# Kernel optimization log

Hardware: AMD Instinct MI355X
Metric: run time of the kernel (lower is better)

The kernel has to match this reference:

```python
import jax, jax.numpy as jnp
import numpy as np

# sizes
B, NA, DEG, TPE = 128, 32, 16, 4
N = B * NA            # 4096 atoms
E = N * DEG           # 65536 edges
T = E * TPE           # 262144 triplets
EA, EE, DT = 128, 128, 64   # atom emb, edge emb, triplet bottleneck
NR, NS, NB = 64, 16, 3      # radial basis, spherical basis, blocks
LAT, HID, NC = 128, 256, 230
CUTOFF, NTYPES = 7.0, 100


def _lattice(lengths, angles):
    """Crystallographic lengths[B,3]/angles[B,3] (deg) -> lattice matrix [B,3,3]."""
    a, b, c = lengths[:, 0], lengths[:, 1], lengths[:, 2]
    al, be, ga = (jnp.deg2rad(angles[:, i]) for i in range(3))
    cos_al, cos_be, cos_ga = jnp.cos(al), jnp.cos(be), jnp.cos(ga)
    sin_ga = jnp.sin(ga)
    zero = jnp.zeros_like(a)
    v1 = jnp.stack([a, zero, zero], -1)
    v2 = jnp.stack([b * cos_ga, b * sin_ga, zero], -1)
    cx = cos_be
    cy = (cos_al - cos_be * cos_ga) / sin_ga
    cz = jnp.sqrt(jnp.clip(1.0 - cx * cx - cy * cy, 1e-8))
    v3 = jnp.stack([c * cx, c * cy, c * cz], -1)
    return jnp.stack([v1, v2, v3], 1)


def setup_inputs() -> dict:
    key = jax.random.key(0)
    ks = jax.random.split(key, 32)

    def w(i, shape, scale=1.0):
        fan_in = shape[-2]
        return scale * jax.random.normal(ks[i], shape, jnp.float32) / np.sqrt(fan_in)

    inp = {
        "noise_levels": jax.random.uniform(ks[0], (B, 1), jnp.float32),
        "frac_coords": jax.random.uniform(ks[1], (N, 3), jnp.float32),
        "lengths": 5.0 + 5.0 * jax.random.uniform(ks[2], (B, 3), jnp.float32),
        "angles": 60.0 + 60.0 * jax.random.uniform(ks[3], (B, 3), jnp.float32),
        "atom_types": jax.random.randint(ks[4], (N,), 0, NTYPES),
        "num_atoms": jnp.full((B,), NA, dtype=jnp.int32),
    }
    # per-crystal random radius graph (no self loops)
    src_l = jax.random.randint(ks[5], (B, NA * DEG), 0, NA)
    dst_l = (src_l + jax.random.randint(ks[6], (B, NA * DEG), 1, NA)) % NA
    off = (jnp.arange(B) * NA)[:, None]
    inp["edge_index"] = jnp.stack([(src_l + off).reshape(-1), (dst_l + off).reshape(-1)]).astype(jnp.int32)
    inp["id3_ji"] = jax.random.randint(ks[7], (T,), 0, E)
    inp["id3_kj"] = jax.random.randint(ks[8], (T,), 0, E)
    # parameters
    inp["atom_emb"] = jax.random.normal(ks[9], (NTYPES, EA), jnp.float32)
    inp["W_hz"] = w(10, (EA + 1, EA))
    inp["W_edge"] = w(11, (2 * EA + NR, EE))
    inp["Wm"] = w(12, (NB, EE, EE))
    inp["Wr1"] = w(13, (NB, NR, EE))
    inp["Wdown"] = w(14, (NB, EE, DT))
    inp["Wcbf"] = w(15, (NB, NS, DT))
    inp["Wup"] = w(16, (NB, DT, EE), 0.5)
    inp["Wa"] = w(17, (NB, EE, EA))
    inp["Wr2"] = w(18, (NB, NR, EA))
    inp["Wh"] = w(19, (NB, EA, EA), 0.5)
    inp["Ws"] = w(20, (NB, EA, EE), 0.5)
    inp["Wt"] = w(21, (NB, EA, EE), 0.5)
    inp["W_out"] = w(22, (EA, LAT))
    inp["W_fc0"] = w(23, (LAT, HID)); inp["b_fc0"] = jnp.zeros((HID,), jnp.float32)
    inp["W_fc1"] = w(24, (HID, HID)); inp["b_fc1"] = jnp.zeros((HID,), jnp.float32)
    inp["W_fc2"] = w(25, (HID, NC)); inp["b_fc2"] = jnp.zeros((NC,), jnp.float32)
    return inp


def reference(noise_levels, frac_coords, lengths, angles, atom_emb, W_hz, W_edge,
              Wm, Wr1, Wdown, Wcbf, Wup, Wa, Wr2, Wh, Ws, Wt, W_out,
              W_fc0, b_fc0, W_fc1, b_fc1, W_fc2, b_fc2,
              atom_types, num_atoms, edge_index, id3_ji, id3_kj):
    silu, seg = jax.nn.silu, jax.ops.segment_sum
    batch = jnp.repeat(jnp.arange(B), num_atoms, total_repeat_length=N)  # [N]
    lat = _lattice(lengths, angles)                                      # [B,3,3]
    pos = jnp.einsum('ni,nij->nj', frac_coords, lat[batch])              # cart coords [N,3]
    src, dst = edge_index[0], edge_index[1]
    vec = pos[dst] - pos[src]                                            # [E,3]
    d = jnp.sqrt(jnp.sum(vec * vec, -1) + 1e-12)
    ds = d / CUTOFF
    # polynomial envelope (p=5) * Bessel radial basis
    env = jnp.where(ds < 1.0, 1.0 - 21.0 * ds**5 + 35.0 * ds**6 - 15.0 * ds**7, 0.0)
    n = jnp.arange(1, NR + 1, dtype=jnp.float32)
    rbf = env[:, None] * np.float32(np.sqrt(2.0 / CUTOFF)) * jnp.sin(n * jnp.pi * ds[:, None]) / d[:, None]  # [E,NR]
    # triplet angles and cosine basis
    v1, v2 = vec[id3_ji], vec[id3_kj]
    cosang = jnp.sum(v1 * v2, -1) / (jnp.linalg.norm(v1, axis=-1) * jnp.linalg.norm(v2, axis=-1) + 1e-9)
    ang = jnp.arccos(jnp.clip(cosang, -1.0 + 1e-6, 1.0 - 1e-6))
    cbf = jnp.cos(jnp.arange(NS, dtype=jnp.float32) * ang[:, None])      # [T,NS]
    # atom embedding conditioned on per-crystal noise level (z, latent_dim=1)
    h = silu(jnp.concatenate([atom_emb[atom_types], noise_levels[batch]], -1) @ W_hz)   # [N,EA]
    m = silu(jnp.concatenate([h[src], h[dst], rbf], -1) @ W_edge)                        # [E,EE]
    for b in range(NB):  # interaction blocks
        x = (silu(m @ Wm[b]) * (rbf @ Wr1[b])) @ Wdown[b]                # [E,DT]
        t = x[id3_kj] * (cbf @ Wcbf[b])                                  # gather + angular modulation [T,DT]
        m = m + silu(seg(t, id3_ji, num_segments=E) @ Wup[b])            # scatter triplets -> edges
        a = seg(silu(m @ Wa[b]) * (rbf @ Wr2[b]), dst, num_segments=N)   # scatter edges -> atoms
        h = h + silu(a @ Wh[b])
        m = m + silu(h[src] @ Ws[b] + h[dst] @ Wt[b])                    # re-embed edges from atoms
    z = seg(h @ W_out, batch, num_segments=B) / num_atoms[:, None].astype(h.dtype)  # [B,LAT] mean pool
    x = jax.nn.relu(z @ W_fc0 + b_fc0)
    x = jax.nn.relu(x @ W_fc1 + b_fc1)
    return x @ W_fc2 + b_fc2                                             # logits [B,NC]
```

## Files before the change

### kernel.cpp

```cpp
#include <hip/hip_runtime.h>
#include <hip/hip_bf16.h>
#include <math.h>

constexpr int B_ = 128, N_ = 4096, E_ = 65536, T_ = 262144;

typedef __attribute__((ext_vector_type(8))) __bf16 bf16x8;
typedef __attribute__((ext_vector_type(4))) float f32x4;
typedef __hip_bfloat16 bf16;

__device__ __forceinline__ float silu_f(float x){ return x / (1.0f + __expf(-x)); }
__device__ __forceinline__ float bf2f(bf16 v){ return __bfloat162float(v); }
__device__ __forceinline__ bf16  f2bf(float v){ return __float2bfloat16(v); }
__device__ __forceinline__ float bfx(bf16x8 v, int j){ __bf16 t = v[j]; return (float)t; }
__device__ __forceinline__ int   swz(int row, int col){ return col ^ ((row & 7) << 3); }

__global__ void hist2_kernel(const int* __restrict__ ji, const int* __restrict__ eidst,
                             int* __restrict__ cnt_ji, int* __restrict__ cnt_dst){
  int i = blockIdx.x*256 + threadIdx.x;
  if(i < T_) atomicAdd(&cnt_ji[ji[i]], 1);
  else       atomicAdd(&cnt_dst[eidst[i - T_]], 1);
}
__global__ void fill2_kernel(const int* __restrict__ ji, const int* __restrict__ eidst,
                             int* __restrict__ cur_ji, int* __restrict__ list_ji,
                             int* __restrict__ cur_dst, int* __restrict__ list_dst){
  int i = blockIdx.x*256 + threadIdx.x;
  if(i < T_){ int p = atomicAdd(&cur_ji[ji[i]], 1); list_ji[p] = i; }
  else { int e = i - T_; int p = atomicAdd(&cur_dst[eidst[e]], 1); list_dst[p] = e; }
}

__global__ __launch_bounds__(256) void scanA_kernel(const int* __restrict__ cnt_ji, const int* __restrict__ cnt_dst,
                                                    int* __restrict__ bsum){
  int blk = blockIdx.x;
  const int* src = (blk < 64) ? cnt_ji : cnt_dst;
  int base = (blk < 64) ? blk*1024 : (blk - 64)*1024;
  int t = threadIdx.x;
  int4 v = *(const int4*)&src[base + t*4];
  int s = v.x + v.y + v.z + v.w;
  #pragma unroll
  for(int d = 1; d < 64; d <<= 1) s += __shfl_xor(s, d);
  __shared__ int ws[4];
  if((t & 63) == 0) ws[t >> 6] = s;
  __syncthreads();
  if(t == 0) bsum[blk] = ws[0] + ws[1] + ws[2] + ws[3];
}
__global__ __launch_bounds__(128) void scanB_kernel(const int* __restrict__ bsum, int* __restrict__ boff){
  __shared__ int sh[68];
  int t = threadIdx.x;
  if(t < 68) sh[t] = bsum[t];
  __syncthreads();
  if(t == 0){
    int run = 0;
    for(int i = 0; i < 64; i++){ boff[i] = run; run += sh[i]; }
    run = 0;
    for(int i = 64; i < 68; i++){ boff[i] = run; run += sh[i]; }
  }
}
__global__ __launch_bounds__(256) void scanC_kernel(const int* __restrict__ cnt_ji, const int* __restrict__ cnt_dst,
                                                    const int* __restrict__ boff,
                                                    int* __restrict__ off_ji, int* __restrict__ cur_ji,
                                                    int* __restrict__ off_dst, int* __restrict__ cur_dst){
  int blk = blockIdx.x;
  const int* src; int* offs; int* cur; int base;
  if(blk < 64){ src = cnt_ji; offs = off_ji; cur = cur_ji; base = blk*1024; }
  else        { src = cnt_dst; offs = off_dst; cur = cur_dst; base = (blk - 64)*1024; }
  int t = threadIdx.x, lane = t & 63, w = t >> 6;
  int4 v = *(const int4*)&src[base + t*4];
  int s4 = v.x + v.y + v.z + v.w;
  int x = s4;
  #pragma unroll
  for(int d = 1; d < 64; d <<= 1){ int u = __shfl_up(x, d); if(lane >= d) x += u; }
  __shared__ int ws[4];
  if(lane == 63) ws[w] = x;
  __syncthreads();
  int wo = 0;
  for(int i = 0; i < w; i++) wo += ws[i];
  int o0 = boff[blk] + wo + (x - s4);
  int4 oo;
  oo.x = o0; oo.y = o0 + v.x; oo.z = oo.y + v.y; oo.w = oo.z + v.z;
  *(int4*)&offs[base + t*4] = oo;
  *(int4*)&cur[base + t*4]  = oo;
  if(blk == 0 && t == 0){ off_ji[E_] = T_; off_dst[N_] = E_; }
}

__global__ void pos_kernel(const float* __restrict__ frac, const float* __restrict__ lengths,
                           const float* __restrict__ angles, float* __restrict__ pos){
  int i = blockIdx.x*256 + threadIdx.x;
  if(i >= N_) return;
  int b = i >> 5;
  const float d2r = 0.017453292519943295f;
  float La = lengths[b*3+0], Lb = lengths[b*3+1], Lc = lengths[b*3+2];
  float al = angles[b*3+0]*d2r, be = angles[b*3+1]*d2r, ga = angles[b*3+2]*d2r;
  float ca = cosf(al), cb = cosf(be), cg = cosf(ga), sg = sinf(ga);
  float cx = cb, cy = (ca - cb*cg) / sg;
  float cz = sqrtf(fmaxf(1.0f - cx*cx - cy*cy, 1e-8f));
  float l00 = La, l10 = Lb*cg, l11 = Lb*sg, l20 = Lc*cx, l21 = Lc*cy, l22 = Lc*cz;
  float fx = frac[i*3], fy = frac[i*3+1], fz = frac[i*3+2];
  pos[i*3+0] = fx*l00 + fy*l10 + fz*l20;
  pos[i*3+1] = fy*l11 + fz*l21;
  pos[i*3+2] = fz*l22;
}

__global__ __launch_bounds__(256) void edge_kernel(const float* __restrict__ pos, const int* __restrict__ ei,
                                                   float* __restrict__ vec, bf16* __restrict__ rbf){
  int e = blockIdx.x*4 + (threadIdx.x >> 6);
  int lane = threadIdx.x & 63;
  int s = ei[e], d = ei[E_ + e];
  float vx = pos[d*3+0]-pos[s*3+0];
  float vy = pos[d*3+1]-pos[s*3+1];
  float vz = pos[d*3+2]-pos[s*3+2];
  float dd = sqrtf(vx*vx + vy*vy + vz*vz + 1e-12f);
  float dsc = dd * (1.0f/7.0f);
  float env = 0.0f;
  if(dsc < 1.0f){
    float d2 = dsc*dsc, d5 = d2*d2*dsc;
    env = 1.0f - 21.0f*d5 + 35.0f*d5*dsc - 15.0f*d5*d2;
  }
  float arg = (float)(lane+1) * 3.14159265358979f * dsc;
  rbf[(size_t)e*64 + lane] = f2bf(env * 0.5345224838248488f * sinf(arg) / dd);
  if(lane < 3){ vec[e*3+lane] = (lane==0) ? vx : (lane==1 ? vy : vz); }
}

__global__ __launch_bounds__(256) void tprep_kernel(const int* __restrict__ list, const int* __restrict__ ji,
                                                    const int* __restrict__ kj, const float* __restrict__ vec,
                                                    bf16* __restrict__ cbf_s, int* __restrict__ kj_s){
  int idx = blockIdx.x*256 + threadIdx.x;
  int t = list[idx];
  int a = ji[t], b = kj[t];
  kj_s[idx] = b;
  float ax = vec[a*3], ay = vec[a*3+1], az = vec[a*3+2];
  float bx = vec[b*3], by = vec[b*3+1], bz = vec[b*3+2];
  float dot = ax*bx + ay*by + az*bz;
  float na = sqrtf(ax*ax + ay*ay + az*az);
  float nb = sqrtf(bx*bx + by*by + bz*bz);
  float x = dot / (na*nb + 1e-9f);
  x = fminf(fmaxf(x, -1.0f + 1e-6f), 1.0f - 1e-6f);
  float c[16];
  c[0] = 1.0f; c[1] = x;
  float x2 = 2.0f * x;
  #pragma unroll
  for(int s = 2; s < 16; s++) c[s] = x2*c[s-1] - c[s-2];
  bf16x8 o0, o1;
  #pragma unroll
  for(int j = 0; j < 8; j++){ o0[j] = (__bf16)c[j]; o1[j] = (__bf16)c[8+j]; }
  *(bf16x8*)&cbf_s[(size_t)idx*16]     = o0;
  *(bf16x8*)&cbf_s[(size_t)idx*16 + 8] = o1;
}

struct WDesc { const float* src; bf16* dst; int K; int shN; };
struct WPackAll { WDesc d[29]; };
__global__ __launch_bounds__(256) void wconv_kernel(WPackAll p){
  WDesc w = p.d[blockIdx.y];
  int idx = blockIdx.x*256 + threadIdx.x;
  int NN = 1 << w.shN;
  if(idx >= w.K * NN) return;
  int k = idx >> w.shN, c = idx & (NN - 1);
  w.dst[(size_t)c * w.K + k] = f2bf(w.src[idx]);
}

__global__ __launch_bounds__(128) void h0_kernel(const float* __restrict__ emb, const int* __restrict__ types,
                                                 const float* __restrict__ noise, const float* __restrict__ Whz,
                                                 float* __restrict__ h, bf16* __restrict__ hbf){
  __shared__ float arow[129];
  int i = blockIdx.x;
  int c = threadIdx.x;
  arow[c] = emb[(size_t)types[i]*128 + c];
  if(c == 0) arow[128] = noise[i >> 5];
  __syncthreads();
  float acc = 0.f;
  for(int k = 0; k < 129; k++) acc += arow[k] * Whz[(size_t)k*128 + c];
  float v = silu_f(acc);
  h[(size_t)i*128 + c] = v;
  hbf[(size_t)i*128 + c] = f2bf(v);
}

template<int KK, int FM>
__device__ __forceinline__ void kloop(const bf16* __restrict__ A, const bf16* __restrict__ W,
                                      int rowA0, int colW0, int lr, int lk, f32x4 (*acc)[4])
{
  #pragma unroll
  for(int k0 = 0; k0 < KK; k0 += 32){
    bf16x8 af[FM], bv[4];
    #pragma unroll
    for(int fm = 0; fm < FM; fm++)
      af[fm] = *(const bf16x8*)(A + (size_t)(rowA0 + fm*16 + lr)*KK + k0 + lk*8);
    #pragma unroll
    for(int fn = 0; fn < 4; fn++)
      bv[fn] = *(const bf16x8*)(W + (size_t)(colW0 + fn*16 + lr)*KK + k0 + lk*8);
    #pragma unroll
    for(int fm = 0; fm < FM; fm++)
      #pragma unroll
      for(int fn = 0; fn < 4; fn++)
        acc[fm][fn] = __builtin_amdgcn_mfma_f32_16x16x32_bf16(af[fm], bv[fn], acc[fm][fn], 0, 0, 0);
  }
}

template<int FM>
__device__ __forceinline__ void kloop_lds(const __bf16* sA, const bf16* __restrict__ W,
                                          int rowL0, int colW0, int lr, int lk, f32x4 (*acc)[4])
{
  #pragma unroll
  for(int k0 = 0; k0 < 128; k0 += 32){
    bf16x8 af[FM], bv[4];
    #pragma unroll
    for(int fm = 0; fm < FM; fm++){
      int row = rowL0 + fm*16 + lr;
      af[fm] = *(const bf16x8*)&sA[row*128 + swz(row, k0 + lk*8)];
    }
    #pragma unroll
    for(int fn = 0; fn < 4; fn++)
      bv[fn] = *(const bf16x8*)(W + (size_t)(colW0 + fn*16 + lr)*128 + k0 + lk*8);
    #pragma unroll
    for(int fm = 0; fm < FM; fm++)
      #pragma unroll
      for(int fn = 0; fn < 4; fn++)
        acc[fm][fn] = __builtin_amdgcn_mfma_f32_16x16x32_bf16(af[fm], bv[fn], acc[fm][fn], 0, 0, 0);
  }
}

__global__ __launch_bounds__(256, 2) void mgemm_m0(
    const bf16* __restrict__ hb, const bf16* __restrict__ rbf, const int* __restrict__ ei,
    const bf16* __restrict__ Wt , bf16* __restrict__ mout)
{
  const int tid = threadIdx.x;
  const int wid = tid >> 6, lane = tid & 63;
  const int wr = wid >> 1, wc = wid & 1;
  const int lr = lane & 15, lk = lane >> 4;
  const int e0 = blockIdx.x*128 + wr*64;

  int esrc[4], edst[4];
  #pragma unroll
  for(int fm = 0; fm < 4; fm++){
    int e = e0 + fm*16 + lr;
    esrc[fm] = ei[e]; edst[fm] = ei[E_ + e];
  }
  f32x4 acc[4][4];
  #pragma unroll
  for(int i = 0; i < 4; i++)
    #pragma unroll
    for(int j = 0; j < 4; j++) acc[i][j] = (f32x4){0.f,0.f,0.f,0.f};

  #pragma unroll
  for(int ks = 0; ks < 10; ks++){
    const int k0 = ks*32;
    bf16x8 af[4], bv[4];
    #pragma unroll
    for(int fm = 0; fm < 4; fm++){
      const bf16* p;
      if(k0 < 128)      p = hb + (size_t)esrc[fm]*128 + k0;
      else if(k0 < 256) p = hb + (size_t)edst[fm]*128 + (k0 - 128);
      else              p = rbf + (size_t)(e0 + fm*16 + lr)*64 + (k0 - 256);
      af[fm] = *(const bf16x8*)(p + lk*8);
    }
    #pragma unroll
    for(int fn = 0; fn < 4; fn++)
      bv[fn] = *(const bf16x8*)(Wt + (size_t)(wc*64 + fn*16 + lr)*320 + k0 + lk*8);
    #pragma unroll
    for(int fm = 0; fm < 4; fm++)
      #pragma unroll
      for(int fn = 0; fn < 4; fn++)
        acc[fm][fn] = __builtin_amdgcn_mfma_f32_16x16x32_bf16(af[fm], bv[fn], acc[fm][fn], 0, 0, 0);
  }
  #pragma unroll
  for(int fm = 0; fm < 4; fm++)
    #pragma unroll
    for(int fn = 0; fn < 4; fn++)
      #pragma unroll
      for(int r = 0; r < 4; r++){
        int row = e0 + fm*16 + lk*4 + r;
        int col = wc*64 + fn*16 + lr;
        mout[(size_t)row*128 + col] = f2bf(silu_f(acc[fm][fn][r]));
      }
}

template<bool SCAT>
__global__ __launch_bounds__(256, 2) void dd_fused(
    bf16* __restrict__ m, const bf16* __restrict__ Wm,
    const bf16* __restrict__ rbf, const bf16* __restrict__ Wr1,
    const bf16* __restrict__ Wd, bf16* __restrict__ xout,
    const int* __restrict__ ei, const bf16* __restrict__ hs, const bf16* __restrict__ ht)
{
  __shared__ __bf16 sM[128*128];
  __shared__ __bf16 sT[128*128];
  const int tid = threadIdx.x;
  const int wid = tid >> 6, lane = tid & 63;
  const int wr = wid >> 1, wc = wid & 1;
  const int lr = lane & 15, lk = lane >> 4;
  const int row0 = blockIdx.x*128;

  {
    int r = tid >> 1, c0 = (tid & 1)*64;
    int e = row0 + r;
    int s = 0, d = 0;
    if(SCAT){ s = ei[e]; d = ei[E_ + e]; }
    #pragma unroll
    for(int j = 0; j < 8; j++){
      int col = c0 + j*8;
      bf16x8 vm = *(const bf16x8*)&m[(size_t)e*128 + col];
      if(SCAT){
        bf16x8 va = *(const bf16x8*)&hs[(size_t)s*128 + col];
        bf16x8 vb = *(const bf16x8*)&ht[(size_t)d*128 + col];
        #pragma unroll
        for(int q = 0; q < 8; q++) vm[q] = (__bf16)(bfx(vm,q) + silu_f(bfx(va,q) + bfx(vb,q)));
        *(bf16x8*)&m[(size_t)e*128 + col] = vm;
      }
      *(bf16x8*)&sM[r*128 + swz(r, col)] = vm;
    }
  }
  __syncthreads();

  f32x4 acc[4][4];
  #pragma unroll
  for(int i = 0; i < 4; i++)
    #pragma unroll
    for(int j = 0; j < 4; j++) acc[i][j] = (f32x4){0.f,0.f,0.f,0.f};
  kloop_lds<4>(sM, Wm, wr*64, wc*64, lr, lk, acc);
  float sv[4][4][4];
  #pragma unroll
  for(int i = 0; i < 4; i++)
    #pragma unroll
    for(int j = 0; j < 4; j++){
      #pragma unroll
      for(int r = 0; r < 4; r++) sv[i][j][r] = silu_f(acc[i][j][r]);
      acc[i][j] = (f32x4){0.f,0.f,0.f,0.f};
    }
  kloop<64,4>(rbf, Wr1, row0 + wr*64, wc*64, lr, lk, acc);

  #pragma unroll
  for(int fm = 0; fm < 4; fm++)
    #pragma unroll
    for(int fn = 0; fn < 4; fn++)
      #pragma unroll
      for(int r = 0; r < 4; r++){
        int row = wr*64 + fm*16 + lk*4 + r;
        int col = wc*64 + fn*16 + lr;
        sT[row*128 + swz(row, col)] = (__bf16)(sv[fm][fn][r] * acc[fm][fn][r]);
      }
  __syncthreads();

  f32x4 a2[2][4];
  #pragma unroll
  for(int i = 0; i < 2; i++)
    #pragma unroll
    for(int j = 0; j < 4; j++) a2[i][j] = (f32x4){0.f,0.f,0.f,0.f};
  kloop_lds<2>(sT, Wd, wid*32, 0, lr, lk, a2);
  #pragma unroll
  for(int fm = 0; fm < 2; fm++)
    #pragma unroll
    for(int fn = 0; fn < 4; fn++)
      #pragma unroll
      for(int r = 0; r < 4; r++){
        int row = wid*32 + fm*16 + lk*4 + r;
        int col = fn*16 + lr;
        xout[(size_t)(row0 + row)*64 + col] = f2bf(a2[fm][fn][r]);
      }
}

template<bool WRITEM>
__global__ __launch_bounds__(256, 2) void wup_wa(
    const bf16* __restrict__ ts, const bf16* __restrict__ Wu,
    bf16* __restrict__ m, const bf16* __restrict__ Wa,
    const bf16* __restrict__ rbf, const bf16* __restrict__ Wr2,
    bf16* __restrict__ tmp)
{
  __shared__ __bf16 sMr[128*128];
  __shared__ __bf16 sU[128*128];
  const int tid = threadIdx.x;
  const int wid = tid >> 6, lane = tid & 63;
  const int wr = wid >> 1, wc = wid & 1;
  const int lr = lane & 15, lk = lane >> 4;
  const int row0 = blockIdx.x*128;

  {
    int r = tid >> 1, c0 = (tid & 1)*64;
    #pragma unroll
    for(int j = 0; j < 8; j++){
      int col = c0 + j*8;
      bf16x8 vm = *(const bf16x8*)&m[(size_t)(row0 + r)*128 + col];
      *(bf16x8*)&sMr[r*128 + swz(r, col)] = vm;
    }
  }
  __syncthreads();

  f32x4 acc[4][4];
  #pragma unroll
  for(int i = 0; i < 4; i++)
    #pragma unroll
    for(int j = 0; j < 4; j++) acc[i][j] = (f32x4){0.f,0.f,0.f,0.f};
  kloop<64,4>(ts, Wu, row0 + wr*64, wc*64, lr, lk, acc);

  #pragma unroll
  for(int fm = 0; fm < 4; fm++)
    #pragma unroll
    for(int fn = 0; fn < 4; fn++)
      #pragma unroll
      for(int r = 0; r < 4; r++){
        int row = wr*64 + fm*16 + lk*4 + r;
        int col = wc*64 + fn*16 + lr;
        float x = (float)sMr[row*128 + swz(row, col)] + silu_f(acc[fm][fn][r]);
        if(WRITEM) m[(size_t)(row0 + row)*128 + col] = f2bf(x);
        sU[row*128 + swz(row, col)] = (__bf16)x;
      }
  __syncthreads();

  #pragma unroll
  for(int i = 0; i < 4; i++)
    #pragma unroll
    for(int j = 0; j < 4; j++) acc[i][j] = (f32x4){0.f,0.f,0.f,0.f};
  kloop_lds<4>(sU, Wa, wr*64, wc*64, lr, lk, acc);
  float sv[4][4][4];
  #pragma unroll
  for(int i = 0; i < 4; i++)
    #pragma unroll
    for(int j = 0; j < 4; j++){
      #pragma unroll
      for(int r = 0; r < 4; r++) sv[i][j][r] = silu_f(acc[i][j][r]);
      acc[i][j] = (f32x4){0.f,0.f,0.f,0.f};
    }
  kloop<64,4>(rbf, Wr2, row0 + wr*64, wc*64, lr, lk, acc);
  #pragma unroll
  for(int fm = 0; fm < 4; fm++)
    #pragma unroll
    for(int fn = 0; fn < 4; fn++)
      #pragma unroll
      for(int r = 0; r < 4; r++){
        int row = wr*64 + fm*16 + lk*4 + r;
        int col = wc*64 + fn*16 + lr;
        tmp[(size_t)(row0 + row)*128 + col] = f2bf(sv[fm][fn][r] * acc[fm][fn][r]);
      }
}

template<bool LAST>
__global__ __launch_bounds__(256, 2) void atom_fused(
    const bf16* __restrict__ a, const bf16* __restrict__ Wh,
    float* __restrict__ h,
    const bf16* __restrict__ Wst, bf16* __restrict__ hs, bf16* __restrict__ ht,
    const bf16* __restrict__ Wo, float* __restrict__ hW)
{
  __shared__ __bf16 sH[128*128];
  const int tid = threadIdx.x;
  const int wid = tid >> 6, lane = tid & 63;
  const int wr = wid >> 1, wc = wid & 1;
  const int lr = lane & 15, lk = lane >> 4;
  const int row0 = blockIdx.x*128;

  f32x4 acc[4][4];
  #pragma unroll
  for(int i = 0; i < 4; i++)
    #pragma unroll
    for(int j = 0; j < 4; j++) acc[i][j] = (f32x4){0.f,0.f,0.f,0.f};
  kloop<128,4>(a, Wh, row0 + wr*64, wc*64, lr, lk, acc);

  #pragma unroll
  for(int fm = 0; fm < 4; fm++)
    #pragma unroll
    for(int fn = 0; fn < 4; fn++)
      #pragma unroll
      for(int r = 0; r < 4; r++){
        int row = wr*64 + fm*16 + lk*4 + r;
        int col = wc*64 + fn*16 + lr;
        size_t off = (size_t)(row0 + row)*128 + col;
        float x = h[off] + silu_f(acc[fm][fn][r]);
        h[off] = x;
        sH[row*128 + swz(row, col)] = (__bf16)x;
      }
  __syncthreads();

  if(!LAST){
    #pragma unroll
    for(int i = 0; i < 4; i++)
      #pragma unroll
      for(int j = 0; j < 4; j++) acc[i][j] = (f32x4){0.f,0.f,0.f,0.f};
    kloop_lds<4>(sH, Wst, wr*64, wc*64, lr, lk, acc);
    #pragma unroll
    for(int fm = 0; fm < 4; fm++)
      #pragma unroll
      for(int fn = 0; fn < 4; fn++)
        #pragma unroll
        for(int r = 0; r < 4; r++){
          int row = wr*64 + fm*16 + lk*4 + r;
          int col = wc*64 + fn*16 + lr;
          hs[(size_t)(row0 + row)*128 + col] = f2bf(acc[fm][fn][r]);
        }
    #pragma unroll
    for(int i = 0; i < 4; i++)
      #pragma unroll
      for(int j = 0; j < 4; j++) acc[i][j] = (f32x4){0.f,0.f,0.f,0.f};
    kloop_lds<4>(sH, Wst + 128*128, wr*64, wc*64, lr, lk, acc);
    #pragma unroll
    for(int fm = 0; fm < 4; fm++)
      #pragma unroll
      for(int fn = 0; fn < 4; fn++)
        #pragma unroll
        for(int r = 0; r < 4; r++){
          int row = wr*64 + fm*16 + lk*4 + r;
          int col = wc*64 + fn*16 + lr;
          ht[(size_t)(row0 + row)*128 + col] = f2bf(acc[fm][fn][r]);
        }
  } else {
    #pragma unroll
    for(int i = 0; i < 4; i++)
      #pragma unroll
      for(int j = 0; j < 4; j++) acc[i][j] = (f32x4){0.f,0.f,0.f,0.f};
    kloop_lds<4>(sH, Wo, wr*64, wc*64, lr, lk, acc);
    #pragma unroll
    for(int fm = 0; fm < 4; fm++)
      #pragma unroll
      for(int fn = 0; fn < 4; fn++)
        #pragma unroll
        for(int r = 0; r < 4; r++){
          int row = wr*64 + fm*16 + lk*4 + r;
          int col = wc*64 + fn*16 + lr;
          hW[(size_t)(row0 + row)*128 + col] = acc[fm][fn][r];
        }
  }
}

__global__ __launch_bounds__(256) void tsum_kernel(const int* __restrict__ offs, const int* __restrict__ kj_s,
                                                   const bf16* __restrict__ cbf_s, const bf16* __restrict__ x,
                                                   const float* __restrict__ Wc, bf16* __restrict__ ts){
  int e = blockIdx.x*4 + (threadIdx.x >> 6);
  int lane = threadIdx.x & 63;
  float wcv[16];
  #pragma unroll
  for(int s = 0; s < 16; s++) wcv[s] = Wc[s*64 + lane];
  float acc = 0.f;
  int b0 = offs[e], b1 = offs[e+1];
  for(int idx = b0; idx < b1; ++idx){
    int k = kj_s[idx];
    bf16x8 c0 = *(const bf16x8*)&cbf_s[(size_t)idx*16];
    bf16x8 c1 = *(const bf16x8*)&cbf_s[(size_t)idx*16 + 8];
    float cw = 0.f;
    #pragma unroll
    for(int j = 0; j < 8; j++) cw += bfx(c0,j)*wcv[j] + bfx(c1,j)*wcv[8+j];
    acc += bf2f(x[(size_t)k*64 + lane]) * cw;
  }
  ts[(size_t)e*64 + lane] = f2bf(acc);
}

__global__ __launch_bounds__(256) void asum_kernel(const int* __restrict__ offs, const int* __restrict__ list,
                                                   const bf16* __restrict__ buf, bf16* __restrict__ a){
  int g = blockIdx.x*256 + threadIdx.x;
  int i = g >> 4, c8 = g & 15;
  float acc[8];
  #pragma unroll
  for(int j = 0; j < 8; j++) acc[j] = 0.f;
  int b0 = offs[i], b1 = offs[i+1];
  for(int idx = b0; idx < b1; ++idx){
    bf16x8 v = *(const bf16x8*)&buf[(size_t)list[idx]*128 + c8*8];
    #pragma unroll
    for(int j = 0; j < 8; j++) acc[j] += bfx(v,j);
  }
  bf16x8 o;
  #pragma unroll
  for(int j = 0; j < 8; j++) o[j] = (__bf16)acc[j];
  *(bf16x8*)&a[(size_t)i*128 + c8*8] = o;
}

__global__ __launch_bounds__(256) void mlp_kernel(const float* __restrict__ hW, const int* __restrict__ numat,
    const float* __restrict__ W0, const float* __restrict__ b0,
    const float* __restrict__ W1, const float* __restrict__ b1,
    const float* __restrict__ W2, const float* __restrict__ b2,
    float* __restrict__ out)
{
  __shared__ float zs[128], x0[256], x1[256];
  int b = blockIdx.x, t = threadIdx.x;
  if(t < 128){
    float s = 0.f;
    #pragma unroll 4
    for(int i = 0; i < 32; i++) s += hW[((size_t)(b*32 + i))*128 + t];
    zs[t] = s / (float)numat[b];
  }
  __syncthreads();
  {
    float acc = b0[t];
    for(int k = 0; k < 128; k++) acc += zs[k] * W0[(size_t)k*256 + t];
    x0[t] = fmaxf(acc, 0.f);
  }
  __syncthreads();
  {
    float acc = b1[t];
    for(int k = 0; k < 256; k++) acc += x0[k] * W1[(size_t)k*256 + t];
    x1[t] = fmaxf(acc, 0.f);
  }
  __syncthreads();
  if(t < 230){
    float acc = b2[t];
    for(int k = 0; k < 256; k++) acc += x1[k] * W2[(size_t)k*230 + t];
    out[(size_t)b*230 + t] = acc;
  }
}

extern "C" void kernel_launch(void* const* d_in, const int* in_sizes, int n_in,
                              void* d_out, int out_size, void* d_ws, size_t ws_size,
                              hipStream_t stream)
{
  const float* noise   = (const float*)d_in[0];
  const float* frac    = (const float*)d_in[1];
  const float* lengths = (const float*)d_in[2];
  const float* angles  = (const float*)d_in[3];
  const int*   types   = (const int*)d_in[4];
  const int*   numat   = (const int*)d_in[5];
  const int*   ei      = (const int*)d_in[6];
  const int*   ji      = (const int*)d_in[7];
  const int*   kj      = (const int*)d_in[8];
  const float* emb     = (const float*)d_in[9];
  const float* Whz     = (const float*)d_in[10];
  const float* Wedge   = (const float*)d_in[11];
  const float* Wm      = (const float*)d_in[12];
  const float* Wr1     = (const float*)d_in[13];
  const float* Wdown   = (const float*)d_in[14];
  const float* Wcbf    = (const float*)d_in[15];
  const float* Wup     = (const float*)d_in[16];
  const float* Wa      = (const float*)d_in[17];
  const float* Wr2     = (const float*)d_in[18];
  const float* Wh      = (const float*)d_in[19];
  const float* Wsw     = (const float*)d_in[20];
  const float* Wtw     = (const float*)d_in[21];
  const float* Wout    = (const float*)d_in[22];
  const float* Wfc0    = (const float*)d_in[23];
  const float* bfc0    = (const float*)d_in[24];
  const float* Wfc1    = (const float*)d_in[25];
  const float* bfc1    = (const float*)d_in[26];
  const float* Wfc2    = (const float*)d_in[27];
  const float* bfc2    = (const float*)d_in[28];
  float* out = (float*)d_out;

  char* base = (char*)d_ws;
  size_t oo = 0;
  auto ab = [&](size_t bytes)->void*{ void* p = base + oo; oo += bytes; oo = (oo + 63) & ~(size_t)63; return p; };

  float* pos   = (float*)ab((size_t)N_*3*4);
  float* vec   = (float*)ab((size_t)E_*3*4);
  bf16*  rbf   = (bf16*) ab((size_t)E_*64*2);
  bf16*  cbf_s = (bf16*) ab((size_t)T_*16*2);
  int*   kj_s  = (int*)  ab((size_t)T_*4);
  float* h     = (float*)ab((size_t)N_*128*4);
  bf16*  hbf   = (bf16*) ab((size_t)N_*128*2);
  bf16*  m     = (bf16*) ab((size_t)E_*128*2);
  bf16*  tmp   = (bf16*) ab((size_t)E_*128*2);
  bf16*  ts    = (bf16*) ab((size_t)E_*64*2);
  bf16*  xbuf  = (bf16*) ab((size_t)E_*64*2);
  bf16*  a     = (bf16*) ab((size_t)N_*128*2);
  bf16*  hsb   = (bf16*) ab((size_t)N_*128*2);
  bf16*  htb   = (bf16*) ab((size_t)N_*128*2);
  float* hW    = (float*)ab((size_t)N_*128*4);

  bf16* WedgeT = (bf16*)ab(320*128*2);
  bf16* WmT    = (bf16*)ab((size_t)3*128*128*2);
  bf16* Wr1T   = (bf16*)ab((size_t)3*128*64*2);
  bf16* WdownT = (bf16*)ab((size_t)3*64*128*2);
  bf16* WupT   = (bf16*)ab((size_t)3*128*64*2);
  bf16* WaT    = (bf16*)ab((size_t)3*128*128*2);
  bf16* Wr2T   = (bf16*)ab((size_t)3*128*64*2);
  bf16* WhT    = (bf16*)ab((size_t)3*128*128*2);
  bf16* WstT   = (bf16*)ab((size_t)3*2*128*128*2);
  bf16* WoutT  = (bf16*)ab(128*128*2);

  int* cnt_ji   = (int*)ab((size_t)(E_ + N_)*4);
  int* cnt_dst  = cnt_ji + E_;
  int* off_ji   = (int*)ab((size_t)(E_+1)*4);
  int* cur_ji   = (int*)ab((size_t)E_*4);
  int* list_ji  = (int*)ab((size_t)T_*4);
  int* off_dst  = (int*)ab((size_t)(N_+1)*4);
  int* cur_dst  = (int*)ab((size_t)N_*4);
  int* list_dst = (int*)ab((size_t)E_*4);
  int* bsum     = (int*)ab(68*4);
  int* boff     = (int*)ab(68*4);

  WPackAll p{};
  {
    int i = 0;
    p.d[i++] = {Wedge, WedgeT, 320, 7};
    for(int b=0;b<3;b++) p.d[i++] = {Wm   + (size_t)b*128*128, WmT   + (size_t)b*128*128, 128, 7};
    for(int b=0;b<3;b++) p.d[i++] = {Wr1  + (size_t)b*64*128,  Wr1T  + (size_t)b*128*64,   64, 7};
    for(int b=0;b<3;b++) p.d[i++] = {Wdown+ (size_t)b*128*64,  WdownT+ (size_t)b*64*128,  128, 6};
    for(int b=0;b<3;b++) p.d[i++] = {Wup  + (size_t)b*64*128,  WupT  + (size_t)b*128*64,   64, 7};
    for(int b=0;b<3;b++) p.d[i++] = {Wa   + (size_t)b*128*128, WaT   + (size_t)b*128*128, 128, 7};
    for(int b=0;b<3;b++) p.d[i++] = {Wr2  + (size_t)b*64*128,  Wr2T  + (size_t)b*128*64,   64, 7};
    for(int b=0;b<3;b++) p.d[i++] = {Wh   + (size_t)b*128*128, WhT   + (size_t)b*128*128, 128, 7};
    for(int b=0;b<3;b++) p.d[i++] = {Wsw  + (size_t)b*128*128, WstT  + (size_t)b*2*128*128,            128, 7};
    for(int b=0;b<3;b++) p.d[i++] = {Wtw  + (size_t)b*128*128, WstT  + (size_t)b*2*128*128 + 128*128,  128, 7};
    p.d[i++] = {Wout, WoutT, 128, 7};
    wconv_kernel<<<dim3(160,29), 256, 0, stream>>>(p);
  }

  hipMemsetAsync(cnt_ji, 0, (size_t)(E_ + N_)*sizeof(int), stream);
  hist2_kernel<<<(T_+E_)/256, 256, 0, stream>>>(ji, ei + E_, cnt_ji, cnt_dst);
  scanA_kernel<<<68, 256, 0, stream>>>(cnt_ji, cnt_dst, bsum);
  scanB_kernel<<<1, 128, 0, stream>>>(bsum, boff);
  scanC_kernel<<<68, 256, 0, stream>>>(cnt_ji, cnt_dst, boff, off_ji, cur_ji, off_dst, cur_dst);
  fill2_kernel<<<(T_+E_)/256, 256, 0, stream>>>(ji, ei + E_, cur_ji, list_ji, cur_dst, list_dst);

  pos_kernel<<<N_/256, 256, 0, stream>>>(frac, lengths, angles, pos);
  edge_kernel<<<E_/4, 256, 0, stream>>>(pos, ei, vec, rbf);
  tprep_kernel<<<T_/256, 256, 0, stream>>>(list_ji, ji, kj, vec, cbf_s, kj_s);
  h0_kernel<<<N_, 128, 0, stream>>>(emb, types, noise, Whz, h, hbf);
  mgemm_m0<<<E_/128, 256, 0, stream>>>(hbf, rbf, ei, WedgeT, m);

  for(int b = 0; b < 3; b++){
    const bf16* WmT_b  = WmT   + (size_t)b*128*128;
    const bf16* Wr1T_b = Wr1T  + (size_t)b*128*64;
    const bf16* WdT_b  = WdownT+ (size_t)b*64*128;
    const float* Wc_b  = Wcbf  + (size_t)b*16*64;
    const bf16* WuT_b  = WupT  + (size_t)b*128*64;
    const bf16* WaT_b  = WaT   + (size_t)b*128*128;
    const bf16* Wr2T_b = Wr2T  + (size_t)b*128*64;
    const bf16* WhT_b  = WhT   + (size_t)b*128*128;
    const bf16* WstT_b = WstT  + (size_t)b*2*128*128;

    if(b == 0) dd_fused<false><<<E_/128, 256, 0, stream>>>(m, WmT_b, rbf, Wr1T_b, WdT_b, xbuf, ei, hsb, htb);
    else       dd_fused<true ><<<E_/128, 256, 0, stream>>>(m, WmT_b, rbf, Wr1T_b, WdT_b, xbuf, ei, hsb, htb);
    tsum_kernel<<<E_/4, 256, 0, stream>>>(off_ji, kj_s, cbf_s, xbuf, Wc_b, ts);
    if(b < 2) wup_wa<true ><<<E_/128, 256, 0, stream>>>(ts, WuT_b, m, WaT_b, rbf, Wr2T_b, tmp);
    else      wup_wa<false><<<E_/128, 256, 0, stream>>>(ts, WuT_b, m, WaT_b, rbf, Wr2T_b, tmp);
    asum_kernel<<<N_*16/256, 256, 0, stream>>>(off_dst, list_dst, tmp, a);
    if(b < 2) atom_fused<false><<<N_/128, 256, 0, stream>>>(a, WhT_b, h, WstT_b, hsb, htb, WoutT, hW);
    else      atom_fused<true ><<<N_/128, 256, 0, stream>>>(a, WhT_b, h, WstT_b, hsb, htb, WoutT, hW);
  }

  mlp_kernel<<<B_, 256, 0, stream>>>(hW, numat, Wfc0, bfc0, Wfc1, bfc1, Wfc2, bfc2, out);
}
```

Before: 608.9 us.

## Fuse triplet prep into CSR fill, fuse edge embedding into first block, halve LDS

Triplet angle and Chebyshev basis computation moves into the CSR fill kernel, which writes sorted kj and fp32 cbf directly, removing the separate tprep pass and the list_ji indirection. The initial edge-embedding GEMM is fused into the first interaction block's down-projection kernel, so m is not re-read from memory. Shared-memory buffers in dd_fused and wup_wa are reused in place, halving LDS per block to raise occupancy. tsum is unrolled by two and reads fp32 cbf, which doubles cbf storage and traffic in exchange for dropping bf16 conversions.

```diff
diff --git a/kernel.cpp b/kernel.cpp
--- a/kernel.cpp
+++ b/kernel.cpp
@@ -20,12 +20,37 @@
   if(i < T_) atomicAdd(&cnt_ji[ji[i]], 1);
   else       atomicAdd(&cnt_dst[eidst[i - T_]], 1);
 }
-__global__ void fill2_kernel(const int* __restrict__ ji, const int* __restrict__ eidst,
-                             int* __restrict__ cur_ji, int* __restrict__ list_ji,
-                             int* __restrict__ cur_dst, int* __restrict__ list_dst){
+
+__global__ __launch_bounds__(256) void fill2t_kernel(const int* __restrict__ ji, const int* __restrict__ kj,
+                                                     const int* __restrict__ eidst, const float* __restrict__ vec,
+                                                     int* __restrict__ cur_ji, int* __restrict__ kj_s,
+                                                     float* __restrict__ cbf_s,
+                                                     int* __restrict__ cur_dst, int* __restrict__ list_dst){
   int i = blockIdx.x*256 + threadIdx.x;
-  if(i < T_){ int p = atomicAdd(&cur_ji[ji[i]], 1); list_ji[p] = i; }
-  else { int e = i - T_; int p = atomicAdd(&cur_dst[eidst[e]], 1); list_dst[p] = e; }
+  if(i < T_){
+    int a = ji[i], b = kj[i];
+    int p = atomicAdd(&cur_ji[a], 1);
+    kj_s[p] = b;
+    float ax = vec[a*3], ay = vec[a*3+1], az = vec[a*3+2];
+    float bx = vec[b*3], by = vec[b*3+1], bz = vec[b*3+2];
+    float dot = ax*bx + ay*by + az*bz;
+    float na = sqrtf(ax*ax + ay*ay + az*az);
+    float nb = sqrtf(bx*bx + by*by + bz*bz);
+    float x = dot / (na*nb + 1e-9f);
+    x = fminf(fmaxf(x, -1.0f + 1e-6f), 1.0f - 1e-6f);
+    float c[16];
+    c[0] = 1.0f; c[1] = x;
+    float x2 = 2.0f * x;
+    #pragma unroll
+    for(int s = 2; s < 16; s++) c[s] = x2*c[s-1] - c[s-2];
+    #pragma unroll
+    for(int q = 0; q < 4; q++)
+      *(float4*)&cbf_s[(size_t)p*16 + q*4] = make_float4(c[q*4], c[q*4+1], c[q*4+2], c[q*4+3]);
+  } else {
+    int e = i - T_;
+    int p = atomicAdd(&cur_dst[eidst[e]], 1);
+    list_dst[p] = e;
+  }
 }
 
 __global__ __launch_bounds__(256) void scanA_kernel(const int* __restrict__ cnt_ji, const int* __restrict__ cnt_dst,
@@ -120,32 +145,6 @@
   if(lane < 3){ vec[e*3+lane] = (lane==0) ? vx : (lane==1 ? vy : vz); }
 }
 
-__global__ __launch_bounds__(256) void tprep_kernel(const int* __restrict__ list, const int* __restrict__ ji,
-                                                    const int* __restrict__ kj, const float* __restrict__ vec,
-                                                    bf16* __restrict__ cbf_s, int* __restrict__ kj_s){
-  int idx = blockIdx.x*256 + threadIdx.x;
-  int t = list[idx];
-  int a = ji[t], b = kj[t];
-  kj_s[idx] = b;
-  float ax = vec[a*3], ay = vec[a*3+1], az = vec[a*3+2];
-  float bx = vec[b*3], by = vec[b*3+1], bz = vec[b*3+2];
-  float dot = ax*bx + ay*by + az*bz;
-  float na = sqrtf(ax*ax + ay*ay + az*az);
-  float nb = sqrtf(bx*bx + by*by + bz*bz);
-  float x = dot / (na*nb + 1e-9f);
-  x = fminf(fmaxf(x, -1.0f + 1e-6f), 1.0f - 1e-6f);
-  float c[16];
-  c[0] = 1.0f; c[1] = x;
-  float x2 = 2.0f * x;
-  #pragma unroll
-  for(int s = 2; s < 16; s++) c[s] = x2*c[s-1] - c[s-2];
-  bf16x8 o0, o1;
-  #pragma unroll
-  for(int j = 0; j < 8; j++){ o0[j] = (__bf16)c[j]; o1[j] = (__bf16)c[8+j]; }
-  *(bf16x8*)&cbf_s[(size_t)idx*16]     = o0;
-  *(bf16x8*)&cbf_s[(size_t)idx*16 + 8] = o1;
-}
-
 struct WDesc { const float* src; bf16* dst; int K; int shN; };
 struct WPackAll { WDesc d[29]; };
 __global__ __launch_bounds__(256) void wconv_kernel(WPackAll p){
@@ -217,15 +216,70 @@
   }
 }
 
-__global__ __launch_bounds__(256, 2) void mgemm_m0(
+__device__ __forceinline__ void dd_tail(__bf16* sM, const bf16* __restrict__ Wm,
+                                        const bf16* __restrict__ rbf, const bf16* __restrict__ Wr1,
+                                        const bf16* __restrict__ Wd, bf16* __restrict__ xout,
+                                        int row0, int wid, int wr, int wc, int lr, int lk)
+{
+  f32x4 acc[4][4];
+  #pragma unroll
+  for(int i = 0; i < 4; i++)
+    #pragma unroll
+    for(int j = 0; j < 4; j++) acc[i][j] = (f32x4){0.f,0.f,0.f,0.f};
+  kloop_lds<4>(sM, Wm, wr*64, wc*64, lr, lk, acc);
+  float sv[4][4][4];
+  #pragma unroll
+  for(int i = 0; i < 4; i++)
+    #pragma unroll
+    for(int j = 0; j < 4; j++){
+      #pragma unroll
+      for(int r = 0; r < 4; r++) sv[i][j][r] = silu_f(acc[i][j][r]);
+      acc[i][j] = (f32x4){0.f,0.f,0.f,0.f};
+    }
+  kloop<64,4>(rbf, Wr1, row0 + wr*64, wc*64, lr, lk, acc);
+  __syncthreads();
+  #pragma unroll
+  for(int fm = 0; fm < 4; fm++)
+    #pragma unroll
+    for(int fn = 0; fn < 4; fn++)
+      #pragma unroll
+      for(int r = 0; r < 4; r++){
+        int row = wr*64 + fm*16 + lk*4 + r;
+        int col = wc*64 + fn*16 + lr;
+        sM[row*128 + swz(row, col)] = (__bf16)(sv[fm][fn][r] * acc[fm][fn][r]);
+      }
+  __syncthreads();
+  f32x4 a2[2][4];
+  #pragma unroll
+  for(int i = 0; i < 2; i++)
+    #pragma unroll
+    for(int j = 0; j < 4; j++) a2[i][j] = (f32x4){0.f,0.f,0.f,0.f};
+  kloop_lds<2>(sM, Wd, wid*32, 0, lr, lk, a2);
+  #pragma unroll
+  for(int fm = 0; fm < 2; fm++)
+    #pragma unroll
+    for(int fn = 0; fn < 4; fn++)
+      #pragma unroll
+      for(int r = 0; r < 4; r++){
+        int row = wid*32 + fm*16 + lk*4 + r;
+        int col = fn*16 + lr;
+        xout[(size_t)(row0 + row)*64 + col] = f2bf(a2[fm][fn][r]);
+      }
+}
+
+__global__ __launch_bounds__(256, 2) void dd0_fused(
     const bf16* __restrict__ hb, const bf16* __restrict__ rbf, const int* __restrict__ ei,
-    const bf16* __restrict__ Wt , bf16* __restrict__ mout)
-{
+    const bf16* __restrict__ We , bf16* __restrict__ m,
+    const bf16* __restrict__ Wm, const bf16* __restrict__ Wr1,
+    const bf16* __restrict__ Wd, bf16* __restrict__ xout)
+{
+  __shared__ __bf16 sM[128*128];
   const int tid = threadIdx.x;
   const int wid = tid >> 6, lane = tid & 63;
   const int wr = wid >> 1, wc = wid & 1;
   const int lr = lane & 15, lk = lane >> 4;
-  const int e0 = blockIdx.x*128 + wr*64;
+  const int row0 = blockIdx.x*128;
+  const int e0 = row0 + wr*64;
 
   int esrc[4], edst[4];
   #pragma unroll
@@ -238,7 +292,6 @@
   for(int i = 0; i < 4; i++)
     #pragma unroll
     for(int j = 0; j < 4; j++) acc[i][j] = (f32x4){0.f,0.f,0.f,0.f};
-
   #pragma unroll
   for(int ks = 0; ks < 10; ks++){
     const int k0 = ks*32;
@@ -253,7 +306,7 @@
     }
     #pragma unroll
     for(int fn = 0; fn < 4; fn++)
-      bv[fn] = *(const bf16x8*)(Wt + (size_t)(wc*64 + fn*16 + lr)*320 + k0 + lk*8);
+      bv[fn] = *(const bf16x8*)(We + (size_t)(wc*64 + fn*16 + lr)*320 + k0 + lk*8);
     #pragma unroll
     for(int fm = 0; fm < 4; fm++)
       #pragma unroll
@@ -266,13 +319,16 @@
     for(int fn = 0; fn < 4; fn++)
       #pragma unroll
       for(int r = 0; r < 4; r++){
-        int row = e0 + fm*16 + lk*4 + r;
+        int row = wr*64 + fm*16 + lk*4 + r;
         int col = wc*64 + fn*16 + lr;
-        mout[(size_t)row*128 + col] = f2bf(silu_f(acc[fm][fn][r]));
+        bf16 v = f2bf(silu_f(acc[fm][fn][r]));
+        m[(size_t)(row0 + row)*128 + col] = v;
+        sM[row*128 + swz(row, col)] = (__bf16)bf2f(v);
       }
-}
-
-template<bool SCAT>
+  __syncthreads();
+  dd_tail(sM, Wm, rbf, Wr1, Wd, xout, row0, wid, wr, wc, lr, lk);
+}
+
 __global__ __launch_bounds__(256, 2) void dd_fused(
     bf16* __restrict__ m, const bf16* __restrict__ Wm,
     const bf16* __restrict__ rbf, const bf16* __restrict__ Wr1,
@@ -280,7 +336,6 @@
     const int* __restrict__ ei, const bf16* __restrict__ hs, const bf16* __restrict__ ht)
 {
   __shared__ __bf16 sM[128*128];
-  __shared__ __bf16 sT[128*128];
   const int tid = threadIdx.x;
   const int wid = tid >> 6, lane = tid & 63;
   const int wr = wid >> 1, wc = wid & 1;
@@ -290,69 +345,21 @@
   {
     int r = tid >> 1, c0 = (tid & 1)*64;
     int e = row0 + r;
-    int s = 0, d = 0;
-    if(SCAT){ s = ei[e]; d = ei[E_ + e]; }
+    int s = ei[e], d = ei[E_ + e];
     #pragma unroll
     for(int j = 0; j < 8; j++){
       int col = c0 + j*8;
       bf16x8 vm = *(const bf16x8*)&m[(size_t)e*128 + col];
-      if(SCAT){
-        bf16x8 va = *(const bf16x8*)&hs[(size_t)s*128 + col];
-        bf16x8 vb = *(const bf16x8*)&ht[(size_t)d*128 + col];
-        #pragma unroll
-        for(int q = 0; q < 8; q++) vm[q] = (__bf16)(bfx(vm,q) + silu_f(bfx(va,q) + bfx(vb,q)));
-        *(bf16x8*)&m[(size_t)e*128 + col] = vm;
-      }
+      bf16x8 va = *(const bf16x8*)&hs[(size_t)s*128 + col];
+      bf16x8 vb = *(const bf16x8*)&ht[(size_t)d*128 + col];
+      #pragma unroll
+      for(int q = 0; q < 8; q++) vm[q] = (__bf16)(bfx(vm,q) + silu_f(bfx(va,q) + bfx(vb,q)));
+      *(bf16x8*)&m[(size_t)e*128 + col] = vm;
       *(bf16x8*)&sM[r*128 + swz(r, col)] = vm;
     }
   }
   __syncthreads();
-
-  f32x4 acc[4][4];
-  #pragma unroll
-  for(int i = 0; i < 4; i++)
-    #pragma unroll
-    for(int j = 0; j < 4; j++) acc[i][j] = (f32x4){0.f,0.f,0.f,0.f};
-  kloop_lds<4>(sM, Wm, wr*64, wc*64, lr, lk, acc);
-  float sv[4][4][4];
-  #pragma unroll
-  for(int i = 0; i < 4; i++)
-    #pragma unroll
-    for(int j = 0; j < 4; j++){
-      #pragma unroll
-      for(int r = 0; r < 4; r++) sv[i][j][r] = silu_f(acc[i][j][r]);
-      acc[i][j] = (f32x4){0.f,0.f,0.f,0.f};
-    }
-  kloop<64,4>(rbf, Wr1, row0 + wr*64, wc*64, lr, lk, acc);
-
-  #pragma unroll
-  for(int fm = 0; fm < 4; fm++)
-    #pragma unroll
-    for(int fn = 0; fn < 4; fn++)
-      #pragma unroll
-      for(int r = 0; r < 4; r++){
-        int row = wr*64 + fm*16 + lk*4 + r;
-        int col = wc*64 + fn*16 + lr;
-        sT[row*128 + swz(row, col)] = (__bf16)(sv[fm][fn][r] * acc[fm][fn][r]);
-      }
-  __syncthreads();
-
-  f32x4 a2[2][4];
-  #pragma unroll
-  for(int i = 0; i < 2; i++)
-    #pragma unroll
-    for(int j = 0; j < 4; j++) a2[i][j] = (f32x4){0.f,0.f,0.f,0.f};
-  kloop_lds<2>(sT, Wd, wid*32, 0, lr, lk, a2);
-  #pragma unroll
-  for(int fm = 0; fm < 2; fm++)
-    #pragma unroll
-    for(int fn = 0; fn < 4; fn++)
-      #pragma unroll
-      for(int r = 0; r < 4; r++){
-        int row = wid*32 + fm*16 + lk*4 + r;
-        int col = fn*16 + lr;
-        xout[(size_t)(row0 + row)*64 + col] = f2bf(a2[fm][fn][r]);
-      }
+  dd_tail(sM, Wm, rbf, Wr1, Wd, xout, row0, wid, wr, wc, lr, lk);
 }
 
 template<bool WRITEM>
@@ -362,8 +369,7 @@
     const bf16* __restrict__ rbf, const bf16* __restrict__ Wr2,
     bf16* __restrict__ tmp)
 {
-  __shared__ __bf16 sMr[128*128];
-  __shared__ __bf16 sU[128*128];
+  __shared__ __bf16 sB[128*128];
   const int tid = threadIdx.x;
   const int wid = tid >> 6, lane = tid & 63;
   const int wr = wid >> 1, wc = wid & 1;
@@ -376,7 +382,7 @@
     for(int j = 0; j < 8; j++){
       int col = c0 + j*8;
       bf16x8 vm = *(const bf16x8*)&m[(size_t)(row0 + r)*128 + col];
-      *(bf16x8*)&sMr[r*128 + swz(r, col)] = vm;
+      *(bf16x8*)&sB[r*128 + swz(r, col)] = vm;
     }
   }
   __syncthreads();
@@ -396,9 +402,9 @@
       for(int r = 0; r < 4; r++){
         int row = wr*64 + fm*16 + lk*4 + r;
         int col = wc*64 + fn*16 + lr;
-        float x = (float)sMr[row*128 + swz(row, col)] + silu_f(acc[fm][fn][r]);
+        float x = (float)sB[row*128 + swz(row, col)] + silu_f(acc[fm][fn][r]);
         if(WRITEM) m[(size_t)(row0 + row)*128 + col] = f2bf(x);
-        sU[row*128 + swz(row, col)] = (__bf16)x;
+        sB[row*128 + swz(row, col)] = (__bf16)x;
       }
   __syncthreads();
 
@@ -406,7 +412,7 @@
   for(int i = 0; i < 4; i++)
     #pragma unroll
     for(int j = 0; j < 4; j++) acc[i][j] = (f32x4){0.f,0.f,0.f,0.f};
-  kloop_lds<4>(sU, Wa, wr*64, wc*64, lr, lk, acc);
+  kloop_lds<4>(sB, Wa, wr*64, wc*64, lr, lk, acc);
   float sv[4][4][4];
   #pragma unroll
   for(int i = 0; i < 4; i++)
@@ -516,7 +522,7 @@
 }
 
 __global__ __launch_bounds__(256) void tsum_kernel(const int* __restrict__ offs, const int* __restrict__ kj_s,
-                                                   const bf16* __restrict__ cbf_s, const bf16* __restrict__ x,
+                                                   const float* __restrict__ cbf_s, const bf16* __restrict__ x,
                                                    const float* __restrict__ Wc, bf16* __restrict__ ts){
   int e = blockIdx.x*4 + (threadIdx.x >> 6);
   int lane = threadIdx.x & 63;
@@ -525,14 +531,28 @@
   for(int s = 0; s < 16; s++) wcv[s] = Wc[s*64 + lane];
   float acc = 0.f;
   int b0 = offs[e], b1 = offs[e+1];
-  for(int idx = b0; idx < b1; ++idx){
-    int k = kj_s[idx];
-    bf16x8 c0 = *(const bf16x8*)&cbf_s[(size_t)idx*16];
-    bf16x8 c1 = *(const bf16x8*)&cbf_s[(size_t)idx*16 + 8];
-    float cw = 0.f;
-    #pragma unroll
-    for(int j = 0; j < 8; j++) cw += bfx(c0,j)*wcv[j] + bfx(c1,j)*wcv[8+j];
-    acc += bf2f(x[(size_t)k*64 + lane]) * cw;
+  int idx = b0;
+  for(; idx + 2 <= b1; idx += 2){
+    int k0 = kj_s[idx], k1 = kj_s[idx+1];
+    float cw0 = 0.f, cw1 = 0.f;
+    #pragma unroll
+    for(int q = 0; q < 4; q++){
+      float4 u = *(const float4*)&cbf_s[(size_t)idx*16 + q*4];
+      float4 v = *(const float4*)&cbf_s[(size_t)(idx+1)*16 + q*4];
+      cw0 += u.x*wcv[q*4] + u.y*wcv[q*4+1] + u.z*wcv[q*4+2] + u.w*wcv[q*4+3];
+      cw1 += v.x*wcv[q*4] + v.y*wcv[q*4+1] + v.z*wcv[q*4+2] + v.w*wcv[q*4+3];
+    }
+    acc += bf2f(x[(size_t)k0*64 + lane]) * cw0 + bf2f(x[(size_t)k1*64 + lane]) * cw1;
+  }
+  if(idx < b1){
+    int k0 = kj_s[idx];
+    float cw0 = 0.f;
+    #pragma unroll
+    for(int q = 0; q < 4; q++){
+      float4 u = *(const float4*)&cbf_s[(size_t)idx*16 + q*4];
+      cw0 += u.x*wcv[q*4] + u.y*wcv[q*4+1] + u.z*wcv[q*4+2] + u.w*wcv[q*4+3];
+    }
+    acc += bf2f(x[(size_t)k0*64 + lane]) * cw0;
   }
   ts[(size_t)e*64 + lane] = f2bf(acc);
 }
@@ -632,7 +652,7 @@
   float* pos   = (float*)ab((size_t)N_*3*4);
   float* vec   = (float*)ab((size_t)E_*3*4);
   bf16*  rbf   = (bf16*) ab((size_t)E_*64*2);
-  bf16*  cbf_s = (bf16*) ab((size_t)T_*16*2);
+  float* cbf_s = (float*)ab((size_t)T_*16*4);
   int*   kj_s  = (int*)  ab((size_t)T_*4);
   float* h     = (float*)ab((size_t)N_*128*4);
   bf16*  hbf   = (bf16*) ab((size_t)N_*128*2);
@@ -660,7 +680,6 @@
   int* cnt_dst  = cnt_ji + E_;
   int* off_ji   = (int*)ab((size_t)(E_+1)*4);
   int* cur_ji   = (int*)ab((size_t)E_*4);
-  int* list_ji  = (int*)ab((size_t)T_*4);
   int* off_dst  = (int*)ab((size_t)(N_+1)*4);
   int* cur_dst  = (int*)ab((size_t)N_*4);
   int* list_dst = (int*)ab((size_t)E_*4);
@@ -689,13 +708,10 @@
   scanA_kernel<<<68, 256, 0, stream>>>(cnt_ji, cnt_dst, bsum);
   scanB_kernel<<<1, 128, 0, stream>>>(bsum, boff);
   scanC_kernel<<<68, 256, 0, stream>>>(cnt_ji, cnt_dst, boff, off_ji, cur_ji, off_dst, cur_dst);
-  fill2_kernel<<<(T_+E_)/256, 256, 0, stream>>>(ji, ei + E_, cur_ji, list_ji, cur_dst, list_dst);
-
   pos_kernel<<<N_/256, 256, 0, stream>>>(frac, lengths, angles, pos);
   edge_kernel<<<E_/4, 256, 0, stream>>>(pos, ei, vec, rbf);
-  tprep_kernel<<<T_/256, 256, 0, stream>>>(list_ji, ji, kj, vec, cbf_s, kj_s);
+  fill2t_kernel<<<(T_+E_)/256, 256, 0, stream>>>(ji, kj, ei + E_, vec, cur_ji, kj_s, cbf_s, cur_dst, list_dst);
   h0_kernel<<<N_, 128, 0, stream>>>(emb, types, noise, Whz, h, hbf);
-  mgemm_m0<<<E_/128, 256, 0, stream>>>(hbf, rbf, ei, WedgeT, m);
 
   for(int b = 0; b < 3; b++){
     const bf16* WmT_b  = WmT   + (size_t)b*128*128;
@@ -708,8 +724,8 @@
     const bf16* WhT_b  = WhT   + (size_t)b*128*128;
     const bf16* WstT_b = WstT  + (size_t)b*2*128*128;
 
-    if(b == 0) dd_fused<false><<<E_/128, 256, 0, stream>>>(m, WmT_b, rbf, Wr1T_b, WdT_b, xbuf, ei, hsb, htb);
-    else       dd_fused<true ><<<E_/128, 256, 0, stream>>>(m, WmT_b, rbf, Wr1T_b, WdT_b, xbuf, ei, hsb, htb);
+    if(b == 0) dd0_fused<<<E_/128, 256, 0, stream>>>(hbf, rbf, ei, WedgeT, m, WmT_b, Wr1T_b, WdT_b, xbuf);
+    else       dd_fused<<<E_/128, 256, 0, stream>>>(m, WmT_b, rbf, Wr1T_b, WdT_b, xbuf, ei, hsb, htb);
     tsum_kernel<<<E_/4, 256, 0, stream>>>(off_ji, kj_s, cbf_s, xbuf, Wc_b, ts);
     if(b < 2) wup_wa<true ><<<E_/128, 256, 0, stream>>>(ts, WuT_b, m, WaT_b, rbf, Wr2T_b, tmp);
     else      wup_wa<false><<<E_/128, 256, 0, stream>>>(ts, WuT_b, m, WaT_b, rbf, Wr2T_b, tmp);
```

New measurement: 659.2 us. 1.08x slower.
